# Performance work log

Hardware: AMD Instinct MI355X
Metric: run time of the kernel (lower is better)

The kernel has to match this reference:

```python
import jax, jax.numpy as jnp
import numpy as np

HIDDEN = 1024
HEADS = 16
HEAD_DIM = HIDDEN // HEADS  # 64
B, S = 4, 2048


def setup_inputs() -> dict:
    key = jax.random.key(0)
    ks = jax.random.split(key, 9)
    sd = 1.0 / np.sqrt(HIDDEN)
    return {
        "hidden_state": jax.random.normal(ks[0], (B, S, HIDDEN), dtype=jnp.float32),
        "Wq": jax.random.uniform(ks[1], (HIDDEN, HIDDEN), jnp.float32, -sd, sd),
        "bq": jax.random.uniform(ks[2], (HIDDEN,), jnp.float32, -sd, sd),
        "Wk": jax.random.uniform(ks[3], (HIDDEN, HEAD_DIM), jnp.float32, -sd, sd),
        "bk": jax.random.uniform(ks[4], (HEAD_DIM,), jnp.float32, -sd, sd),
        "Wv": jax.random.uniform(ks[5], (HIDDEN, HEAD_DIM), jnp.float32, -sd, sd),
        "bv": jax.random.uniform(ks[6], (HEAD_DIM,), jnp.float32, -sd, sd),
        "Wo": jax.random.uniform(ks[7], (HIDDEN, HIDDEN), jnp.float32, -sd, sd),
        "bo": jax.random.uniform(ks[8], (HIDDEN,), jnp.float32, -sd, sd),
    }


def reference(hidden_state, Wq, bq, Wk, bk, Wv, bv, Wo, bo):
    b, s, _ = hidden_state.shape
    # projections
    q = hidden_state @ Wq + bq               # [B,S,H*Dh]
    k = hidden_state @ Wk + bk               # [B,S,Dh] (shared across heads)
    v = hidden_state @ Wv + bv               # [B,S,Dh]
    q = q.reshape(b, s, HEADS, HEAD_DIM)     # [B,S,H,Dh]
    scale = 1.0 / jnp.sqrt(jnp.float32(HEAD_DIM))
    # scores: [B,H,S,S] — shared K broadcast over heads via einsum
    scores = jnp.einsum("bqhd,bkd->bhqk", q, k) * scale
    probs = jax.nn.softmax(scores, axis=-1)
    out = jnp.einsum("bhqk,bkd->bqhd", probs, v)  # [B,S,H,Dh]
    out = out.reshape(b, s, HEADS * HEAD_DIM)
    return out @ Wo + bo
```

## Files before the change

### kernel.cpp

```cpp
#include <hip/hip_runtime.h>
#include <hip/hip_bf16.h>
#include <cstdint>

#define HIDDEN 1024
#define HEADS 16
#define HEAD_DIM 64
#define BB 4
#define SS 2048
#define NTOK (BB * SS)

typedef __attribute__((ext_vector_type(8))) __bf16 bf16x8;
typedef __attribute__((ext_vector_type(4))) float f32x4;
typedef unsigned short u16;

#define PSCALE 0.1803368801111137f

__device__ __forceinline__ u16 f2bf(float x) {
    union { float f; uint32_t u; } v; v.f = x;
    uint32_t r = v.u + 0x7FFF + ((v.u >> 16) & 1);
    return (u16)(r >> 16);
}

typedef __attribute__((address_space(3))) uint32_t lds_u32;
typedef __attribute__((address_space(1))) uint32_t glb_u32;
__device__ __forceinline__ void gload16(const u16* g, u16* l) {
    __builtin_amdgcn_global_load_lds((const glb_u32*)g, (lds_u32*)l, 16, 0, 0);
}

__global__ void cvt_f32_bf16(const float* __restrict__ in, u16* __restrict__ out, int n4) {
    int i = blockIdx.x * blockDim.x + threadIdx.x;
    int stride = gridDim.x * blockDim.x;
    for (; i < n4; i += stride) {
        float4 v = ((const float4*)in)[i];
        ushort4 o;
        o.x = f2bf(v.x); o.y = f2bf(v.y); o.z = f2bf(v.z); o.w = f2bf(v.w);
        ((ushort4*)out)[i] = o;
    }
}

__global__ void transpose4_to_bf16(const float* __restrict__ Wq, const float* __restrict__ Wk,
                                   const float* __restrict__ Wv, const float* __restrict__ Wo,
                                   u16* __restrict__ Wta, u16* __restrict__ Wot) {
    __shared__ float tile[32][33];
    const int z = blockIdx.z;
    const int Nz = (z == 1 || z == 2) ? 64 : 1024;
    const int bx = blockIdx.x;
    if (bx * 32 >= Nz) return;
    const float* W = (z == 0) ? Wq : (z == 1) ? Wk : (z == 2) ? Wv : Wo;
    u16* Wt = (z == 0) ? Wta : (z == 1) ? (Wta + (size_t)1024 * HIDDEN)
              : (z == 2) ? (Wta + (size_t)1088 * HIDDEN) : Wot;
    const int by = blockIdx.y;
    const int tx = threadIdx.x;
    const int ty = threadIdx.y;
    for (int i = 0; i < 4; i++) {
        int kk = ty + i * 8;
        tile[kk][tx] = W[(size_t)(by * 32 + kk) * Nz + bx * 32 + tx];
    }
    __syncthreads();
    for (int i = 0; i < 4; i++) {
        int nn = ty + i * 8;
        Wt[(size_t)(bx * 32 + nn) * 1024 + by * 32 + tx] = f2bf(tile[tx][nn]);
    }
}

__global__ __launch_bounds__(256) void gemm128_f32(
    const u16* __restrict__ A, const u16* __restrict__ Bt,
    const float* __restrict__ bias, float* __restrict__ C,
    int M, int N, int K) {
    __shared__ u16 Al[128 * 64];
    __shared__ u16 Bl[128 * 64];
    const int mb = blockIdx.y, nb = blockIdx.x;
    const int tid = threadIdx.x;
    const int w = tid >> 6, lane = tid & 63;
    const int lr = lane & 15, lg = lane >> 4;
    const int wr = w >> 1, wc = w & 1;

    f32x4 acc[4][4] = {};

    const int srow = lane >> 3;
    const int scol = (lane & 7) * 8;
    const u16* Asrc = A + (size_t)(mb * 128 + w * 32 + srow) * K + scol;
    const u16* Bsrc = Bt + (size_t)(nb * 128 + w * 32 + srow) * K + scol;
    u16* Adst = &Al[(w * 32) * 64];
    u16* Bdst = &Bl[(w * 32) * 64];

    for (int k0 = 0; k0 < K; k0 += 64) {
        if (k0) __syncthreads();
#pragma unroll
        for (int i = 0; i < 4; i++) {
            gload16(Asrc + (size_t)(i * 8) * K + k0, Adst + i * 8 * 64);
            gload16(Bsrc + (size_t)(i * 8) * K + k0, Bdst + i * 8 * 64);
        }
        asm volatile("s_waitcnt vmcnt(0)" ::: "memory");
        __syncthreads();

#pragma unroll
        for (int ks = 0; ks < 2; ks++) {
            bf16x8 af[4], bfr[4];
#pragma unroll
            for (int mf = 0; mf < 4; mf++)
                af[mf] = *(const bf16x8*)(&Al[(wr * 64 + mf * 16 + lr) * 64 + ks * 32 + lg * 8]);
#pragma unroll
            for (int nf = 0; nf < 4; nf++)
                bfr[nf] = *(const bf16x8*)(&Bl[(wc * 64 + nf * 16 + lr) * 64 + ks * 32 + lg * 8]);
            __builtin_amdgcn_s_setprio(1);
#pragma unroll
            for (int mf = 0; mf < 4; mf++)
#pragma unroll
                for (int nf = 0; nf < 4; nf++)
                    acc[mf][nf] = __builtin_amdgcn_mfma_f32_16x16x32_bf16(af[mf], bfr[nf], acc[mf][nf], 0, 0, 0);
            __builtin_amdgcn_s_setprio(0);
        }
    }

#pragma unroll
    for (int nf = 0; nf < 4; nf++) {
        int n = nb * 128 + wc * 64 + nf * 16 + lr;
        float bval = bias[n];
#pragma unroll
        for (int mf = 0; mf < 4; mf++)
#pragma unroll
            for (int r = 0; r < 4; r++) {
                int m = mb * 128 + wr * 64 + mf * 16 + lg * 4 + r;
                C[(size_t)m * N + n] = acc[mf][nf][r] + bval;
            }
    }
}

#define NPROJ 1152
__global__ __launch_bounds__(256) void gemm_proj(
    const u16* __restrict__ A, const u16* __restrict__ Bt,
    const float* __restrict__ bq, const float* __restrict__ bk, const float* __restrict__ bv,
    u16* __restrict__ qout, u16* __restrict__ kout, u16* __restrict__ vout) {
    __shared__ u16 Al[128 * 64];
    __shared__ u16 Bl[128 * 64];
    const int mb = blockIdx.y, nb = blockIdx.x;
    const int tid = threadIdx.x;
    const int w = tid >> 6, lane = tid & 63;
    const int lr = lane & 15, lg = lane >> 4;
    const int wr = w >> 1, wc = w & 1;

    f32x4 acc[4][4] = {};

    const int srow = lane >> 3;
    const int scol = (lane & 7) * 8;
    const u16* Asrc = A + (size_t)(mb * 128 + w * 32 + srow) * HIDDEN + scol;
    const u16* Bsrc = Bt + (size_t)(nb * 128 + w * 32 + srow) * HIDDEN + scol;
    u16* Adst = &Al[(w * 32) * 64];
    u16* Bdst = &Bl[(w * 32) * 64];

    for (int k0 = 0; k0 < HIDDEN; k0 += 64) {
        if (k0) __syncthreads();
#pragma unroll
        for (int i = 0; i < 4; i++) {
            gload16(Asrc + (size_t)(i * 8) * HIDDEN + k0, Adst + i * 8 * 64);
            gload16(Bsrc + (size_t)(i * 8) * HIDDEN + k0, Bdst + i * 8 * 64);
        }
        asm volatile("s_waitcnt vmcnt(0)" ::: "memory");
        __syncthreads();

#pragma unroll
        for (int ks = 0; ks < 2; ks++) {
            bf16x8 af[4], bfr[4];
#pragma unroll
            for (int mf = 0; mf < 4; mf++)
                af[mf] = *(const bf16x8*)(&Al[(wr * 64 + mf * 16 + lr) * 64 + ks * 32 + lg * 8]);
#pragma unroll
            for (int nf = 0; nf < 4; nf++)
                bfr[nf] = *(const bf16x8*)(&Bl[(wc * 64 + nf * 16 + lr) * 64 + ks * 32 + lg * 8]);
            __builtin_amdgcn_s_setprio(1);
#pragma unroll
            for (int mf = 0; mf < 4; mf++)
#pragma unroll
                for (int nf = 0; nf < 4; nf++)
                    acc[mf][nf] = __builtin_amdgcn_mfma_f32_16x16x32_bf16(af[mf], bfr[nf], acc[mf][nf], 0, 0, 0);
            __builtin_amdgcn_s_setprio(0);
        }
    }

#pragma unroll
    for (int nf = 0; nf < 4; nf++) {
        int n = nb * 128 + wc * 64 + nf * 16 + lr;
        float bval = (n < 1024) ? bq[n] : (n < 1088) ? bk[n - 1024] : bv[n - 1088];
#pragma unroll
        for (int mf = 0; mf < 4; mf++)
#pragma unroll
            for (int r = 0; r < 4; r++) {
                int m = mb * 128 + wr * 64 + mf * 16 + lg * 4 + r;
                float val = acc[mf][nf][r] + bval;
                if (n < 1024) {
                    qout[(size_t)m * 1024 + n] = f2bf(val * PSCALE);
                } else if (n < 1088) {
                    kout[(size_t)m * 64 + (n - 1024)] = f2bf(val);
                } else {
                    int bb = m >> 11, t = m & (SS - 1);
                    vout[((size_t)bb * 64 + (n - 1088)) * SS + t] = f2bf(val);
                }
            }
    }
}

#define KVB 64
#define NT (SS / KVB)

__global__ __launch_bounds__(512) void attn_kernel(
    const u16* __restrict__ q,
    const u16* __restrict__ k,
    const u16* __restrict__ vt,
    u16* __restrict__ o) {
    const int qt = blockIdx.x, h = blockIdx.y, b = blockIdx.z;
    const int tid = threadIdx.x;
    const int w = tid >> 6, lane = tid & 63;
    const int lr = lane & 15, lg = lane >> 4;

    __shared__ u16 Kl[4][KVB * 64];
    __shared__ u16 Vl[4][KVB * 64];

    const u16* kbase = k + (size_t)b * SS * HEAD_DIM;
    const u16* vbase = vt + (size_t)b * HEAD_DIM * SS;
    const int rowbase = b * SS + qt * 256 + w * 32;

    const int srow = w * 8 + (lane >> 3);
    const int sc16 = (lane & 7) ^ (srow & 7);
    const u16* kp = kbase + (size_t)srow * HEAD_DIM + sc16 * 8;
    const u16* vp = vbase + (size_t)srow * SS + sc16 * 8;

    bf16x8 qf[2][2];
#pragma unroll
    for (int s = 0; s < 2; s++)
#pragma unroll
        for (int ks = 0; ks < 2; ks++)
            qf[s][ks] = *(const bf16x8*)(q + (size_t)(rowbase + s * 16 + lr) * HIDDEN + h * 64 + ks * 32 + lg * 8);

    bf16x8 onesf;
#pragma unroll
    for (int i = 0; i < 8; i++) onesf[i] = (__bf16)1.0f;

    const int xr = lr & 7;
    const int kvro0 = lr * 64 + ((lg) ^ xr) * 8;
    const int kvro1 = lr * 64 + ((4 + lg) ^ xr) * 8;

    f32x4 l_acc[2] = {};
    f32x4 oacc[2][4] = {};
    uint32_t pw[16];

#define VEXP(D, S) asm("v_exp_f32 %0, %1" : "=v"(D) : "v"(S))

#define STAGE(BUF)                            \
    do {                                      \
        gload16(kp, &Kl[BUF][w * 512]);       \
        gload16(vp, &Vl[BUF][w * 512]);       \
        kp += KVB * HEAD_DIM;                 \
        vp += KVB;                            \
    } while (0)

#define QKEXP(BUF)                                                                     \
    do {                                                                               \
        f32x4 st0[4] = {}, st1[4] = {};                                                \
        __builtin_amdgcn_s_setprio(1);                                                 \
        _Pragma("unroll") for (int nf = 0; nf < 4; nf++) {                             \
            bf16x8 kf = *(const bf16x8*)(&Kl[BUF][kvro0 + nf * 1024]);                 \
            st0[nf] = __builtin_amdgcn_mfma_f32_16x16x32_bf16(kf, qf[0][0], st0[nf], 0, 0, 0); \
            st1[nf] = __builtin_amdgcn_mfma_f32_16x16x32_bf16(kf, qf[1][0], st1[nf], 0, 0, 0); \
        }                                                                              \
        _Pragma("unroll") for (int nf = 0; nf < 4; nf++) {                             \
            bf16x8 kf = *(const bf16x8*)(&Kl[BUF][kvro1 + nf * 1024]);                 \
            st0[nf] = __builtin_amdgcn_mfma_f32_16x16x32_bf16(kf, qf[0][1], st0[nf], 0, 0, 0); \
            st1[nf] = __builtin_amdgcn_mfma_f32_16x16x32_bf16(kf, qf[1][1], st1[nf], 0, 0, 0); \
        }                                                                              \
        __builtin_amdgcn_s_setprio(0);                                                 \
        uint32_t c0[8], c1[8];                                                         \
        _Pragma("unroll") for (int nf = 0; nf < 4; nf++) {                             \
            float p0, p1, p2, p3, r0, r1, r2, r3;                                      \
            VEXP(p0, st0[nf][0]); VEXP(p1, st0[nf][1]);                                \
            VEXP(p2, st0[nf][2]); VEXP(p3, st0[nf][3]);                                \
            asm("v_cvt_pk_bf16_f32 %0, %1, %2" : "=v"(c0[nf * 2]) : "v"(p0), "v"(p1)); \
            asm("v_cvt_pk_bf16_f32 %0, %1, %2" : "=v"(c0[nf * 2 + 1]) : "v"(p2), "v"(p3)); \
            VEXP(r0, st1[nf][0]); VEXP(r1, st1[nf][1]);                                \
            VEXP(r2, st1[nf][2]); VEXP(r3, st1[nf][3]);                                \
            asm("v_cvt_pk_bf16_f32 %0, %1, %2" : "=v"(c1[nf * 2]) : "v"(r0), "v"(r1)); \
            asm("v_cvt_pk_bf16_f32 %0, %1, %2" : "=v"(c1[nf * 2 + 1]) : "v"(r2), "v"(r3)); \
        }                                                                              \
        _Pragma("unroll") for (int ks = 0; ks < 2; ks++) {                             \
            uint32_t u0 = c0[4 * ks], v0 = c0[4 * ks + 1], x0 = c0[4 * ks + 2], y0 = c0[4 * ks + 3]; \
            uint32_t u1 = c1[4 * ks], v1 = c1[4 * ks + 1], x1 = c1[4 * ks + 2], y1 = c1[4 * ks + 3]; \
            asm("v_permlane32_swap_b32 %0, %1" : "+v"(u0), "+v"(x0));                  \
            asm("v_permlane32_swap_b32 %0, %1" : "+v"(v0), "+v"(y0));                  \
            asm("v_permlane16_swap_b32 %0, %1" : "+v"(u0), "+v"(x0));                  \
            asm("v_permlane16_swap_b32 %0, %1" : "+v"(v0), "+v"(y0));                  \
            asm("v_permlane32_swap_b32 %0, %1" : "+v"(u1), "+v"(x1));                  \
            asm("v_permlane32_swap_b32 %0, %1" : "+v"(v1), "+v"(y1));                  \
            asm("v_permlane16_swap_b32 %0, %1" : "+v"(u1), "+v"(x1));                  \
            asm("v_permlane16_swap_b32 %0, %1" : "+v"(v1), "+v"(y1));                  \
            pw[ks * 4 + 0] = u0; pw[ks * 4 + 1] = v0;                                  \
            pw[ks * 4 + 2] = x0; pw[ks * 4 + 3] = y0;                                  \
            pw[8 + ks * 4 + 0] = u1; pw[8 + ks * 4 + 1] = v1;                          \
            pw[8 + ks * 4 + 2] = x1; pw[8 + ks * 4 + 3] = y1;                          \
        }                                                                              \
    } while (0)

#define PVACC(BUF)                                                                     \
    do {                                                                               \
        union { uint32_t wv[4]; bf16x8 v8; } pf0, pf1;                                 \
        __builtin_amdgcn_s_setprio(1);                                                 \
        _Pragma("unroll") for (int ks = 0; ks < 2; ks++) {                             \
            pf0.wv[0] = pw[ks * 4 + 0]; pf0.wv[1] = pw[ks * 4 + 1];                    \
            pf0.wv[2] = pw[ks * 4 + 2]; pf0.wv[3] = pw[ks * 4 + 3];                    \
            pf1.wv[0] = pw[8 + ks * 4 + 0]; pf1.wv[1] = pw[8 + ks * 4 + 1];            \
            pf1.wv[2] = pw[8 + ks * 4 + 2]; pf1.wv[3] = pw[8 + ks * 4 + 3];            \
            const int kvro = ks ? kvro1 : kvro0;                                       \
            l_acc[0] = __builtin_amdgcn_mfma_f32_16x16x32_bf16(pf0.v8, onesf, l_acc[0], 0, 0, 0); \
            l_acc[1] = __builtin_amdgcn_mfma_f32_16x16x32_bf16(pf1.v8, onesf, l_acc[1], 0, 0, 0); \
            _Pragma("unroll") for (int nf = 0; nf < 4; nf++) {                         \
                bf16x8 vf = *(const bf16x8*)(&Vl[BUF][kvro + nf * 1024]);              \
                oacc[0][nf] = __builtin_amdgcn_mfma_f32_16x16x32_bf16(pf0.v8, vf, oacc[0][nf], 0, 0, 0); \
                oacc[1][nf] = __builtin_amdgcn_mfma_f32_16x16x32_bf16(pf1.v8, vf, oacc[1][nf], 0, 0, 0); \
            }                                                                          \
        }                                                                              \
        __builtin_amdgcn_s_setprio(0);                                                 \
    } while (0)

#define ITER(BPV, BQK, BST, DOSTAGE, VM)                           \
    do {                                                           \
        asm volatile("s_waitcnt vmcnt(" #VM ")" ::: "memory");     \
        __builtin_amdgcn_s_barrier();                              \
        if (DOSTAGE) STAGE(BST);                                   \
        PVACC(BPV);                                                \
        QKEXP(BQK);                                                \
        asm volatile("" ::: "memory");                             \
    } while (0)

    STAGE(0);
    STAGE(1);
    asm volatile("s_waitcnt vmcnt(2)" ::: "memory");
    __builtin_amdgcn_s_barrier();
    STAGE(2);
    QKEXP(0);

    for (int i = 0; i < 7; i++) {
        ITER(0, 1, 3, 1, 2);
        ITER(1, 2, 0, 1, 2);
        ITER(2, 3, 1, 1, 2);
        ITER(3, 0, 2, 1, 2);
    }
    ITER(0, 1, 3, 1, 2);
    ITER(1, 2, 3, 0, 2);
    ITER(2, 3, 3, 0, 0);
    PVACC(3);

#undef ITER
#undef STAGE
#undef QKEXP
#undef PVACC
#undef VEXP

#pragma unroll
    for (int s = 0; s < 2; s++) {
        float li[4];
#pragma unroll
        for (int r = 0; r < 4; r++) li[r] = 1.0f / l_acc[s][r];
#pragma unroll
        for (int nf = 0; nf < 4; nf++)
#pragma unroll
            for (int r = 0; r < 4; r++) {
                float val = oacc[s][nf][r] * li[r];
                o[(size_t)(rowbase + s * 16 + lg * 4 + r) * HIDDEN + h * 64 + nf * 16 + lr] = f2bf(val);
            }
    }
}

extern "C" void kernel_launch(void* const* d_in, const int* in_sizes, int n_in,
                              void* d_out, int out_size, void* d_ws, size_t ws_size,
                              hipStream_t stream) {
    const float* h  = (const float*)d_in[0];
    const float* Wq = (const float*)d_in[1];
    const float* bq = (const float*)d_in[2];
    const float* Wk = (const float*)d_in[3];
    const float* bk = (const float*)d_in[4];
    const float* Wv = (const float*)d_in[5];
    const float* bv = (const float*)d_in[6];
    const float* Wo = (const float*)d_in[7];
    const float* bo = (const float*)d_in[8];

    char* ws = (char*)d_ws;
    u16* hbf  = (u16*)ws; ws += (size_t)NTOK * HIDDEN * 2;
    u16* Wta  = (u16*)ws; ws += (size_t)NPROJ * HIDDEN * 2;
    u16* Wot  = (u16*)ws; ws += (size_t)HIDDEN * HIDDEN * 2;
    u16* qbf  = (u16*)ws; ws += (size_t)NTOK * HIDDEN * 2;
    u16* kbf  = (u16*)ws; ws += (size_t)NTOK * HEAD_DIM * 2;
    u16* vtb  = (u16*)ws; ws += (size_t)NTOK * HEAD_DIM * 2;
    u16* obf  = (u16*)ws; ws += (size_t)NTOK * HIDDEN * 2;

    cvt_f32_bf16<<<2048, 256, 0, stream>>>(h, hbf, NTOK * HIDDEN / 4);
    transpose4_to_bf16<<<dim3(32, 32, 4), dim3(32, 8), 0, stream>>>(Wq, Wk, Wv, Wo, Wta, Wot);

    gemm_proj<<<dim3(NPROJ / 128, NTOK / 128), 256, 0, stream>>>(hbf, Wta, bq, bk, bv, qbf, kbf, vtb);

    attn_kernel<<<dim3(SS / 256, HEADS, BB), 512, 0, stream>>>(qbf, kbf, vtb, obf);

    gemm128_f32<<<dim3(HIDDEN / 128, NTOK / 128), 256, 0, stream>>>(obf, Wot, bo, (float*)d_out, NTOK, HIDDEN, HIDDEN);
}
```

Baseline: 146.1 us.

## Double-buffer LDS tiles in projection and output GEMMs to overlap loads

Both GEMM kernels now use two LDS buffers, issuing global-to-LDS loads for the next K tile right after the barrier and then computing on the current tile. This drops one barrier per iteration and hides global load latency behind MFMA work. The loop is hardcoded for K=1024 via macros, and LDS use per block doubles to 64KB, which may lower occupancy.

```diff
diff --git a/kernel.cpp b/kernel.cpp
--- a/kernel.cpp
+++ b/kernel.cpp
@@ -63,56 +63,70 @@
     }
 }
 
+
+#define GEMM_PRE(APTR, BPTR)                                                         \
+    __shared__ u16 Al[2][128 * 64];                                                  \
+    __shared__ u16 Bl[2][128 * 64];                                                  \
+    const int mb = blockIdx.y, nb = blockIdx.x;                                      \
+    const int tid = threadIdx.x;                                                     \
+    const int w = tid >> 6, lane = tid & 63;                                         \
+    const int lr = lane & 15, lg = lane >> 4;                                        \
+    const int wr = w >> 1, wc = w & 1;                                               \
+    f32x4 acc[4][4] = {};                                                            \
+    const int srow = lane >> 3;                                                      \
+    const int scol = (lane & 7) * 8;                                                 \
+    const u16* Ap = APTR + (size_t)(mb * 128 + w * 32 + srow) * 1024 + scol;         \
+    const u16* Bp = BPTR + (size_t)(nb * 128 + w * 32 + srow) * 1024 + scol;
+
+#define GSTAGE(BUF)                                                                  \
+    do {                                                                             \
+        _Pragma("unroll") for (int i = 0; i < 4; i++) {                              \
+            gload16(Ap + (size_t)(i * 8) * 1024, &Al[BUF][(w * 32 + i * 8) * 64]);   \
+            gload16(Bp + (size_t)(i * 8) * 1024, &Bl[BUF][(w * 32 + i * 8) * 64]);   \
+        }                                                                            \
+        Ap += 64;                                                                    \
+        Bp += 64;                                                                    \
+    } while (0)
+
+#define GCOMPUTE(BUF)                                                                \
+    do {                                                                             \
+        _Pragma("unroll") for (int ks = 0; ks < 2; ks++) {                           \
+            bf16x8 af[4], bfr[4];                                                    \
+            _Pragma("unroll") for (int mf = 0; mf < 4; mf++)                         \
+                af[mf] = *(const bf16x8*)(&Al[BUF][(wr * 64 + mf * 16 + lr) * 64 + ks * 32 + lg * 8]); \
+            _Pragma("unroll") for (int nf = 0; nf < 4; nf++)                         \
+                bfr[nf] = *(const bf16x8*)(&Bl[BUF][(wc * 64 + nf * 16 + lr) * 64 + ks * 32 + lg * 8]); \
+            __builtin_amdgcn_s_setprio(1);                                           \
+            _Pragma("unroll") for (int mf = 0; mf < 4; mf++)                         \
+                _Pragma("unroll") for (int nf = 0; nf < 4; nf++)                     \
+                    acc[mf][nf] = __builtin_amdgcn_mfma_f32_16x16x32_bf16(af[mf], bfr[nf], acc[mf][nf], 0, 0, 0); \
+            __builtin_amdgcn_s_setprio(0);                                           \
+        }                                                                            \
+    } while (0)
+
+#define GITER(BUF, DOSTAGE)                                        \
+    do {                                                           \
+        asm volatile("s_waitcnt vmcnt(0)" ::: "memory");           \
+        __builtin_amdgcn_s_barrier();                              \
+        if (DOSTAGE) GSTAGE(BUF ^ 1);                              \
+        GCOMPUTE(BUF);                                             \
+        asm volatile("" ::: "memory");                             \
+    } while (0)
+
+#define GEMM_LOOP()                                                \
+    GSTAGE(0);                                                     \
+    for (int i = 0; i < 7; i++) {                                  \
+        GITER(0, 1);                                               \
+        GITER(1, 1);                                               \
+    }                                                              \
+    GITER(0, 1);                                                   \
+    GITER(1, 0);
+
 __global__ __launch_bounds__(256) void gemm128_f32(
     const u16* __restrict__ A, const u16* __restrict__ Bt,
-    const float* __restrict__ bias, float* __restrict__ C,
-    int M, int N, int K) {
-    __shared__ u16 Al[128 * 64];
-    __shared__ u16 Bl[128 * 64];
-    const int mb = blockIdx.y, nb = blockIdx.x;
-    const int tid = threadIdx.x;
-    const int w = tid >> 6, lane = tid & 63;
-    const int lr = lane & 15, lg = lane >> 4;
-    const int wr = w >> 1, wc = w & 1;
-
-    f32x4 acc[4][4] = {};
-
-    const int srow = lane >> 3;
-    const int scol = (lane & 7) * 8;
-    const u16* Asrc = A + (size_t)(mb * 128 + w * 32 + srow) * K + scol;
-    const u16* Bsrc = Bt + (size_t)(nb * 128 + w * 32 + srow) * K + scol;
-    u16* Adst = &Al[(w * 32) * 64];
-    u16* Bdst = &Bl[(w * 32) * 64];
-
-    for (int k0 = 0; k0 < K; k0 += 64) {
-        if (k0) __syncthreads();
-#pragma unroll
-        for (int i = 0; i < 4; i++) {
-            gload16(Asrc + (size_t)(i * 8) * K + k0, Adst + i * 8 * 64);
-            gload16(Bsrc + (size_t)(i * 8) * K + k0, Bdst + i * 8 * 64);
-        }
-        asm volatile("s_waitcnt vmcnt(0)" ::: "memory");
-        __syncthreads();
-
-#pragma unroll
-        for (int ks = 0; ks < 2; ks++) {
-            bf16x8 af[4], bfr[4];
-#pragma unroll
-            for (int mf = 0; mf < 4; mf++)
-                af[mf] = *(const bf16x8*)(&Al[(wr * 64 + mf * 16 + lr) * 64 + ks * 32 + lg * 8]);
-#pragma unroll
-            for (int nf = 0; nf < 4; nf++)
-                bfr[nf] = *(const bf16x8*)(&Bl[(wc * 64 + nf * 16 + lr) * 64 + ks * 32 + lg * 8]);
-            __builtin_amdgcn_s_setprio(1);
-#pragma unroll
-            for (int mf = 0; mf < 4; mf++)
-#pragma unroll
-                for (int nf = 0; nf < 4; nf++)
-                    acc[mf][nf] = __builtin_amdgcn_mfma_f32_16x16x32_bf16(af[mf], bfr[nf], acc[mf][nf], 0, 0, 0);
-            __builtin_amdgcn_s_setprio(0);
-        }
-    }
-
+    const float* __restrict__ bias, float* __restrict__ C, int N) {
+    GEMM_PRE(A, Bt);
+    GEMM_LOOP();
 #pragma unroll
     for (int nf = 0; nf < 4; nf++) {
         int n = nb * 128 + wc * 64 + nf * 16 + lr;
@@ -132,52 +146,8 @@
     const u16* __restrict__ A, const u16* __restrict__ Bt,
     const float* __restrict__ bq, const float* __restrict__ bk, const float* __restrict__ bv,
     u16* __restrict__ qout, u16* __restrict__ kout, u16* __restrict__ vout) {
-    __shared__ u16 Al[128 * 64];
-    __shared__ u16 Bl[128 * 64];
-    const int mb = blockIdx.y, nb = blockIdx.x;
-    const int tid = threadIdx.x;
-    const int w = tid >> 6, lane = tid & 63;
-    const int lr = lane & 15, lg = lane >> 4;
-    const int wr = w >> 1, wc = w & 1;
-
-    f32x4 acc[4][4] = {};
-
-    const int srow = lane >> 3;
-    const int scol = (lane & 7) * 8;
-    const u16* Asrc = A + (size_t)(mb * 128 + w * 32 + srow) * HIDDEN + scol;
-    const u16* Bsrc = Bt + (size_t)(nb * 128 + w * 32 + srow) * HIDDEN + scol;
-    u16* Adst = &Al[(w * 32) * 64];
-    u16* Bdst = &Bl[(w * 32) * 64];
-
-    for (int k0 = 0; k0 < HIDDEN; k0 += 64) {
-        if (k0) __syncthreads();
-#pragma unroll
-        for (int i = 0; i < 4; i++) {
-            gload16(Asrc + (size_t)(i * 8) * HIDDEN + k0, Adst + i * 8 * 64);
-            gload16(Bsrc + (size_t)(i * 8) * HIDDEN + k0, Bdst + i * 8 * 64);
-        }
-        asm volatile("s_waitcnt vmcnt(0)" ::: "memory");
-        __syncthreads();
-
-#pragma unroll
-        for (int ks = 0; ks < 2; ks++) {
-            bf16x8 af[4], bfr[4];
-#pragma unroll
-            for (int mf = 0; mf < 4; mf++)
-                af[mf] = *(const bf16x8*)(&Al[(wr * 64 + mf * 16 + lr) * 64 + ks * 32 + lg * 8]);
-#pragma unroll
-            for (int nf = 0; nf < 4; nf++)
-                bfr[nf] = *(const bf16x8*)(&Bl[(wc * 64 + nf * 16 + lr) * 64 + ks * 32 + lg * 8]);
-            __builtin_amdgcn_s_setprio(1);
-#pragma unroll
-            for (int mf = 0; mf < 4; mf++)
-#pragma unroll
-                for (int nf = 0; nf < 4; nf++)
-                    acc[mf][nf] = __builtin_amdgcn_mfma_f32_16x16x32_bf16(af[mf], bfr[nf], acc[mf][nf], 0, 0, 0);
-            __builtin_amdgcn_s_setprio(0);
-        }
-    }
-
+    GEMM_PRE(A, Bt);
+    GEMM_LOOP();
 #pragma unroll
     for (int nf = 0; nf < 4; nf++) {
         int n = nb * 128 + wc * 64 + nf * 16 + lr;
@@ -398,5 +368,5 @@
 
     attn_kernel<<<dim3(SS / 256, HEADS, BB), 512, 0, stream>>>(qbf, kbf, vtb, obf);
 
-    gemm128_f32<<<dim3(HIDDEN / 128, NTOK / 128), 256, 0, stream>>>(obf, Wot, bo, (float*)d_out, NTOK, HIDDEN, HIDDEN);
-}
+    gemm128_f32<<<dim3(HIDDEN / 128, NTOK / 128), 256, 0, stream>>>(obf, Wot, bo, (float*)d_out, HIDDEN);
+}
```

New measurement: 155.0 us. +6.1%, slower.
